# Optimization experiments

Measured on AMD Instinct MI355X. Metric: run time of the kernel, lower is better.

The kernel has to match this reference:

```python
import jax, jax.numpy as jnp
import numpy as np

EPS = 1e-5

def setup_inputs() -> dict:
    key = jax.random.key(0)
    k1, k2, k3 = jax.random.split(key, 3)
    x = jax.random.normal(k1, (16, 256, 32, 32), dtype=jnp.float32)
    embed = jax.random.normal(k2, (8192, 256), dtype=jnp.float32)
    cluster_size = jax.random.uniform(k3, (8192,), dtype=jnp.float32)
    return {"x": x, "embed": embed, "cluster_size": cluster_size}

def reference(x, embed, cluster_size):
    # x: (b, c, h, w) -> (b, h*w, c); project_in is Identity (codebook_dim == dim, heads=1)
    b, c, h, w = x.shape
    xt = jnp.transpose(x, (0, 2, 3, 1)).reshape(b, h * w, c)   # (b, n, d)
    flat = xt.reshape(-1, c)                                    # (N, d)
    d2 = (jnp.sum(flat * flat, axis=1, keepdims=True)
          - 2.0 * flat @ embed.T
          + jnp.sum(embed * embed, axis=1))                     # (N, K)
    embed_ind_flat = jnp.argmin(d2, axis=-1)                    # (N,) temperature==0 -> argmax of -d2
    quantize = embed[embed_ind_flat].reshape(b, h * w, c)       # gather codebook rows
    embed_ind = embed_ind_flat.reshape(b, h * w)
    # perplexity over (unnormalized) EMA cluster sizes, as in the torch code
    probs = cluster_size
    perplexity = jnp.exp(-jnp.sum(probs * jnp.log(probs + EPS)))
    # eval-mode commitment loss (weight_loss=True, commitment_weight=1.0)
    commit_loss = jnp.mean((quantize - xt) ** 2)
    return quantize, embed_ind, perplexity, commit_loss
```

## Files before the change

kernel.cpp:

```cpp
#include <hip/hip_runtime.h>
#include <hip/hip_bf16.h>
#include <math.h>

typedef _Float16 f16x8 __attribute__((ext_vector_type(8)));
typedef float f32x4 __attribute__((ext_vector_type(4)));

#define N_TOK 16384
#define D 256
#define K 8192

#define Q_OFF 0
#define IND_OFF 4194304
#define PERP_OFF 4210688
#define COMMIT_OFF 4210689

#define WS_CAND   0u
#define WS_E2     1048576u
#define WS_DSUM   1081344u
#define WS_EH     1114112u
#define WS_XH     5308416u
#define WS_XT     13697024u
#define WS_NEED   30474240u

__device__ __forceinline__ unsigned int ford(float f) {
    unsigned int u = __float_as_uint(f);
    return (u & 0x80000000u) ? ~u : (u | 0x80000000u);
}
__device__ __forceinline__ unsigned short f2h(float f) {
    _Float16 h = (_Float16)f;
    return *(unsigned short*)&h;
}
__device__ __forceinline__ void gload16(const void* g, void* l) {
    __builtin_amdgcn_global_load_lds(
        (const __attribute__((address_space(1))) unsigned int*)g,
        (__attribute__((address_space(3))) unsigned int*)l, 16, 0, 0);
}


__global__ void vq_convert_x(const float* __restrict__ x, float* __restrict__ xt,
                             unsigned short* __restrict__ xh) {
    __shared__ float t[64][65];
    const int tid = threadIdx.x;
    const int p0 = blockIdx.x * 64, c0 = blockIdx.y * 64, b = blockIdx.z;
    const int q = tid & 15, h = tid >> 4;
    #pragma unroll
    for (int r = 0; r < 4; ++r) {
        const int cl = r * 16 + h;
        const float4 v = *(const float4*)(x + (((size_t)(b * 256 + c0 + cl)) << 10) + p0 + q * 4);
        t[cl][q * 4 + 0] = v.x; t[cl][q * 4 + 1] = v.y;
        t[cl][q * 4 + 2] = v.z; t[cl][q * 4 + 3] = v.w;
    }
    __syncthreads();
    #pragma unroll
    for (int r = 0; r < 4; ++r) {
        const int nl = r * 16 + h;
        const int n = (b << 10) + p0 + nl;
        const int c = c0 + q * 4;
        float4 vf; ushort4 vh;
        vf.x = t[q * 4 + 0][nl]; vf.y = t[q * 4 + 1][nl];
        vf.z = t[q * 4 + 2][nl]; vf.w = t[q * 4 + 3][nl];
        vh.x = f2h(vf.x); vh.y = f2h(vf.y); vh.z = f2h(vf.z); vh.w = f2h(vf.w);
        *(float4*)(xt + ((size_t)n << 8) + c) = vf;
        *(ushort4*)(xh + ((size_t)n << 8) + c) = vh;
    }
}

__global__ void vq_prep_e(const float* __restrict__ e, unsigned short* __restrict__ eh,
                          float* __restrict__ e2, double* __restrict__ dsum) {
    if (blockIdx.x == 0 && threadIdx.x == 0) *dsum = 0.0;
    const int wave = threadIdx.x >> 6, lane = threadIdx.x & 63;
    const int c = blockIdx.x * 4 + wave;
    const float4 v = *(const float4*)(e + (size_t)c * D + lane * 4);
    ushort4 vh;
    vh.x = f2h(v.x); vh.y = f2h(v.y); vh.z = f2h(v.z); vh.w = f2h(v.w);
    *(ushort4*)(eh + (size_t)c * D + lane * 4) = vh;
    float s = v.x * v.x + v.y * v.y + v.z * v.z + v.w * v.w;
    #pragma unroll
    for (int off = 32; off > 0; off >>= 1) s += __shfl_down(s, off, 64);
    if (lane == 0) e2[c] = s;
}

__global__ __launch_bounds__(256, 2) void vq_mfma_kernel(
    const unsigned short* __restrict__ xh, const unsigned short* __restrict__ eh,
    const float* __restrict__ e2, unsigned int* __restrict__ cand) {
    __shared__ __align__(16) unsigned short Bs[2][32 * 64];

    const int tid = threadIdx.x;
    const int lane = tid & 63, wid = tid >> 6;
    const int l15 = lane & 15, lg = lane >> 4;
    const int split = blockIdx.y;
    const int m0 = blockIdx.x * 256;
    const int c0s = split * 1024;
    const int rw = m0 + wid * 64;

    f16x8 a[4][8];
    #pragma unroll
    for (int mf = 0; mf < 4; ++mf) {
        const unsigned short* ap = xh + (((size_t)(rw + mf * 16 + l15)) << 8) + lg * 8;
        #pragma unroll
        for (int t = 0; t < 8; ++t)
            a[mf][t] = *(const f16x8*)(ap + t * 32);
    }

    {
        const int r = tid >> 3, cl = tid & 7;
        gload16(eh + (((size_t)(c0s + r)) << 8) + ((cl ^ (r & 7)) << 3),
                (char*)Bs[0] + tid * 16);
    }

    int boff[2][2];
    #pragma unroll
    for (int nf = 0; nf < 2; ++nf)
        #pragma unroll
        for (int ks2 = 0; ks2 < 2; ++ks2) {
            const int rb = nf * 16 + l15;
            boff[nf][ks2] = rb * 128 + (((ks2 * 4 + lg) ^ (rb & 7)) << 4);
        }

    float d1[16], d2[16];
    unsigned int ipk[16];
    #pragma unroll
    for (int r = 0; r < 16; ++r) { d1[r] = INFINITY; d2[r] = INFINITY; ipk[r] = 0; }

    __syncthreads();

    #pragma unroll 1
    for (int ct = 0; ct < 32; ++ct) {
        const int c0 = c0s + ct * 32;
        float e2v0 = e2[c0 + l15];
        float e2v1 = e2[c0 + 16 + l15];
        f32x4 acc[4][2];
        #pragma unroll
        for (int mf = 0; mf < 4; ++mf) {
            f32x4 z = {0.f, 0.f, 0.f, 0.f};
            acc[mf][0] = z; acc[mf][1] = z;
        }
        #pragma unroll
        for (int ks = 0; ks < 4; ++ks) {
            const int s = ct * 4 + ks;
            const int cur = s & 1;
            if (s < 127) {
                const int s1 = s + 1;
                const int c0n = c0s + (s1 >> 2) * 32;
                const int kkn = (s1 & 3) * 64;
                const int r = tid >> 3, cl = tid & 7;
                gload16(eh + (((size_t)(c0n + r)) << 8) + kkn + ((cl ^ (r & 7)) << 3),
                        (char*)Bs[cur ^ 1] + tid * 16);
            }
            #pragma unroll
            for (int ks2 = 0; ks2 < 2; ++ks2) {
                const f16x8 b0 = *(const f16x8*)((const char*)Bs[cur] + boff[0][ks2]);
                const f16x8 b1 = *(const f16x8*)((const char*)Bs[cur] + boff[1][ks2]);
                #pragma unroll
                for (int mf = 0; mf < 4; ++mf) {
                    acc[mf][0] = __builtin_amdgcn_mfma_f32_16x16x32_f16(
                        a[mf][ks * 2 + ks2], b0, acc[mf][0], 0, 0, 0);
                    acc[mf][1] = __builtin_amdgcn_mfma_f32_16x16x32_f16(
                        a[mf][ks * 2 + ks2], b1, acc[mf][1], 0, 0, 0);
                }
            }
            __syncthreads();
        }
        const unsigned int cl0 = (unsigned int)(ct * 32 + l15);
        #pragma unroll
        for (int mf = 0; mf < 4; ++mf) {
            #pragma unroll
            for (int reg = 0; reg < 4; ++reg) {
                const int rr = mf * 4 + reg;
                const float sc0 = fmaf(-2.0f, acc[mf][0][reg], e2v0);
                const float sc1 = fmaf(-2.0f, acc[mf][1][reg], e2v1);
                if (fminf(sc0, sc1) < d2[rr]) {
                    {
                        const bool lt1 = sc0 < d1[rr], lt2 = sc0 < d2[rr];
                        const unsigned int ii = ipk[rr];
                        const unsigned int nif = (ii << 16) | cl0;
                        const unsigned int nis = (ii & 0xFFFFu) | (cl0 << 16);
                        d2[rr] = lt1 ? d1[rr] : (lt2 ? sc0 : d2[rr]);
                        ipk[rr] = lt1 ? nif : (lt2 ? nis : ii);
                        d1[rr] = lt1 ? sc0 : d1[rr];
                    }
                    {
                        const unsigned int cl1 = cl0 + 16;
                        const bool lt1 = sc1 < d1[rr], lt2 = sc1 < d2[rr];
                        const unsigned int ii = ipk[rr];
                        const unsigned int nif = (ii << 16) | cl1;
                        const unsigned int nis = (ii & 0xFFFFu) | (cl1 << 16);
                        d2[rr] = lt1 ? d1[rr] : (lt2 ? sc1 : d2[rr]);
                        ipk[rr] = lt1 ? nif : (lt2 ? nis : ii);
                        d1[rr] = lt1 ? sc1 : d1[rr];
                    }
                }
            }
        }
    }

    unsigned long long p1[16], p2[16];
    #pragma unroll
    for (int r = 0; r < 16; ++r) {
        p1[r] = (((unsigned long long)ford(d1[r])) << 32) |
                (unsigned int)(c0s + (ipk[r] & 0xFFFFu));
        p2[r] = (((unsigned long long)ford(d2[r])) << 32) |
                (unsigned int)(c0s + (ipk[r] >> 16));
    }
    #pragma unroll
    for (int st = 1; st < 16; st <<= 1) {
        #pragma unroll
        for (int r = 0; r < 16; ++r) {
            const unsigned long long q1 = __shfl_xor(p1[r], st, 64);
            const unsigned long long q2 = __shfl_xor(p2[r], st, 64);
            const unsigned long long n1 = p1[r] < q1 ? p1[r] : q1;
            const unsigned long long hi = p1[r] < q1 ? q1 : p1[r];
            const unsigned long long l2 = p2[r] < q2 ? p2[r] : q2;
            p1[r] = n1;
            p2[r] = hi < l2 ? hi : l2;
        }
    }
    if (l15 == 0) {
        #pragma unroll
        for (int mf = 0; mf < 4; ++mf)
            #pragma unroll
            for (int reg = 0; reg < 4; ++reg) {
                const int n = rw + mf * 16 + lg * 4 + reg;
                unsigned int* cp = cand + (((size_t)n) << 4) + split * 2;
                cp[0] = (unsigned int)p1[mf * 4 + reg];
                cp[1] = (unsigned int)p2[mf * 4 + reg];
            }
    }
}

__global__ void vq_rescore_finalize(const float* __restrict__ xt, const float* __restrict__ embed,
                                    const float* __restrict__ e2,
                                    const unsigned int* __restrict__ cand,
                                    float* __restrict__ out, double* __restrict__ dsum) {
    __shared__ double red[4];
    const int tid = threadIdx.x, wid = tid >> 6, lane = tid & 63;
    double wsum = 0.0;
    #pragma unroll 1
    for (int it = 0; it < 8; ++it) {
        const int n = blockIdx.x * 32 + it * 4 + wid;
        const float4 xv = *(const float4*)(xt + (((size_t)n) << 8) + lane * 4);
        unsigned long long best = 0xFFFFFFFFFFFFFFFFull;
        #pragma unroll 2
        for (int j = 0; j < 16; ++j) {
            const unsigned int c = cand[(((size_t)n) << 4) + j];
            const float4 ev = *(const float4*)(embed + (((size_t)c) << 8) + lane * 4);
            float dt = xv.x * ev.x + xv.y * ev.y + xv.z * ev.z + xv.w * ev.w;
            #pragma unroll
            for (int off = 32; off > 0; off >>= 1) dt += __shfl_xor(dt, off, 64);
            const float s = fmaf(-2.0f, dt, e2[c]);
            const unsigned long long p = (((unsigned long long)ford(s)) << 32) | c;
            best = p < best ? p : best;
        }
        const unsigned int bi = (unsigned int)(best & 0xFFFFFFFFull);
        if (lane == 0) out[IND_OFF + n] = (float)bi;
        const float4 ev = *(const float4*)(embed + (((size_t)bi) << 8) + lane * 4);
        *(float4*)(out + Q_OFF + (((size_t)n) << 8) + lane * 4) = ev;
        const float q0 = ev.x - xv.x, q1 = ev.y - xv.y, q2 = ev.z - xv.z, q3 = ev.w - xv.w;
        float a4 = q0 * q0 + q1 * q1 + q2 * q2 + q3 * q3;
        #pragma unroll
        for (int off = 32; off > 0; off >>= 1) a4 += __shfl_xor(a4, off, 64);
        if (lane == 0) wsum += (double)a4;
    }
    if (lane == 0) red[wid] = wsum;
    __syncthreads();
    if (tid == 0) atomicAdd(dsum, red[0] + red[1] + red[2] + red[3]);
}

__global__ void vq_tail_kernel(const float* __restrict__ cs,
                               const double* __restrict__ dsum,
                               float* __restrict__ out) {
    __shared__ double red[4];
    const int tid = threadIdx.x;
    double s = 0.0;
    for (int i = tid; i < K; i += 256) {
        const float p = cs[i];
        s += (double)(p * logf(p + 1e-5f));
    }
    #pragma unroll
    for (int off = 32; off > 0; off >>= 1) s += __shfl_down(s, off, 64);
    if ((tid & 63) == 0) red[tid >> 6] = s;
    __syncthreads();
    if (tid == 0) {
        const double tot = red[0] + red[1] + red[2] + red[3];
        const double pv = exp(-tot);
        out[PERP_OFF] = (pv > 3.3e38) ? 3.3e38f : (float)pv;
        out[COMMIT_OFF] = (float)(*dsum * (1.0 / 4194304.0));
    }
}

#define TM 64
#define TN 64
#define BKF 32
#define NSPLITF 2
#define CODES_PER_SPLIT (K / NSPLITF)
#define TILES_PER_SPLIT (CODES_PER_SPLIT / TN)

__global__ void vq_init_kernel(unsigned long long* __restrict__ keys, double* __restrict__ dsum) {
    int i = blockIdx.x * blockDim.x + threadIdx.x;
    if (i < N_TOK) keys[i] = 0xFFFFFFFFFFFFFFFFull;
    if (i == 0) *dsum = 0.0;
}
__global__ void vq_e2_kernel(const float* __restrict__ embed, float* __restrict__ e2) {
    int wave = threadIdx.x >> 6, lane = threadIdx.x & 63;
    int c = blockIdx.x * 4 + wave;
    const float4 v = *(const float4*)(embed + (size_t)c * D + lane * 4);
    float s = v.x * v.x + v.y * v.y + v.z * v.z + v.w * v.w;
    #pragma unroll
    for (int off = 32; off > 0; off >>= 1) s += __shfl_down(s, off, 64);
    if (lane == 0) e2[c] = s;
}
__global__ __launch_bounds__(256, 2) void vq_argmin_kernel(
    const float* __restrict__ x, const float* __restrict__ embed,
    const float* __restrict__ e2, unsigned long long* __restrict__ keys) {
    __shared__ float xT[D][TM];
    __shared__ float eT[BKF][TN + 4];
    const int tid = threadIdx.x;
    const int n0 = blockIdx.x * TM;
    const int b = n0 >> 10, p0 = n0 & 1023;
    const float* xb = x + (size_t)b * D * 1024 + p0;
    {
        const int t4 = (tid & 15) * 4, chb = tid >> 4;
        #pragma unroll
        for (int pass = 0; pass < 16; ++pass) {
            const int ch = pass * 16 + chb;
            *(float4*)&xT[ch][t4] = *(const float4*)(xb + (size_t)ch * 1024 + t4);
        }
    }
    __syncthreads();
    const int tm4 = (tid & 15) * 4, tn = tid >> 4, tn4 = tn * 4;
    float bestd[4]; int besti[4];
    #pragma unroll
    for (int i = 0; i < 4; ++i) { bestd[i] = INFINITY; besti[i] = 0x7fffffff; }
    for (int ct = 0; ct < TILES_PER_SPLIT; ++ct) {
        const int c0 = blockIdx.y * CODES_PER_SPLIT + ct * TN;
        float acc[4][4] = {};
        for (int kk = 0; kk < D; kk += BKF) {
            {
                const int j = tid >> 2, ch4 = (tid & 3) * 4;
                #pragma unroll
                for (int p = 0; p < 2; ++p) {
                    const int chl = p * 16 + ch4;
                    const float4 ev = *(const float4*)(embed + (size_t)(c0 + j) * D + kk + chl);
                    eT[chl + 0][j] = ev.x; eT[chl + 1][j] = ev.y;
                    eT[chl + 2][j] = ev.z; eT[chl + 3][j] = ev.w;
                }
            }
            __syncthreads();
            #pragma unroll
            for (int k2 = 0; k2 < BKF; ++k2) {
                const float4 a = *(const float4*)&xT[kk + k2][tm4];
                const float4 bv = *(const float4*)&eT[k2][tn4];
                acc[0][0] += a.x * bv.x; acc[0][1] += a.x * bv.y; acc[0][2] += a.x * bv.z; acc[0][3] += a.x * bv.w;
                acc[1][0] += a.y * bv.x; acc[1][1] += a.y * bv.y; acc[1][2] += a.y * bv.z; acc[1][3] += a.y * bv.w;
                acc[2][0] += a.z * bv.x; acc[2][1] += a.z * bv.y; acc[2][2] += a.z * bv.z; acc[2][3] += a.z * bv.w;
                acc[3][0] += a.w * bv.x; acc[3][1] += a.w * bv.y; acc[3][2] += a.w * bv.z; acc[3][3] += a.w * bv.w;
            }
            __syncthreads();
        }
        #pragma unroll
        for (int j = 0; j < 4; ++j) {
            const int c = c0 + tn4 + j;
            const float ec = e2[c];
            #pragma unroll
            for (int i = 0; i < 4; ++i) {
                const float s = ec - 2.0f * acc[i][j];
                if (s < bestd[i]) { bestd[i] = s; besti[i] = c; }
            }
        }
    }
    __syncthreads();
    float* cd = &eT[0][0];
    int* ci = (int*)&eT[16][0];
    #pragma unroll
    for (int i = 0; i < 4; ++i) { cd[tn * 64 + tm4 + i] = bestd[i]; ci[tn * 64 + tm4 + i] = besti[i]; }
    __syncthreads();
    if (tid < TM) {
        float bd = INFINITY; int bi = 0x7fffffff;
        for (int j = 0; j < 16; ++j) {
            const float d = cd[j * 64 + tid]; const int idx = ci[j * 64 + tid];
            if (d < bd || (d == bd && idx < bi)) { bd = d; bi = idx; }
        }
        atomicMin(&keys[n0 + tid], (((unsigned long long)ford(bd)) << 32) | (unsigned int)bi);
    }
}
__global__ void vq_finalize_kernel(const float* __restrict__ x, const float* __restrict__ embed,
                                   const unsigned long long* __restrict__ keys,
                                   float* __restrict__ out, double* __restrict__ dsum) {
    const int tid = threadIdx.x;
    const int n0 = blockIdx.x * 64;
    const int t = tid >> 2, q = tid & 3;
    const int n = n0 + t;
    const int b = n >> 10, p = n & 1023;
    if (tid < 64) {
        const int nn = n0 + tid;
        out[IND_OFF + nn] = (float)(int)(unsigned int)(keys[nn] & 0xFFFFFFFFull);
    }
    const int idx = (int)(unsigned int)(keys[n] & 0xFFFFFFFFull);
    const float* erow = embed + (size_t)idx * D;
    const float* xrow = x + (size_t)b * D * 1024 + p;
    float* qrow = out + Q_OFF + (size_t)n * D;
    float acc = 0.0f;
    #pragma unroll
    for (int i = 0; i < 16; ++i) {
        const int ch = i * 16 + q * 4;
        const float4 ev = *(const float4*)(erow + ch);
        *(float4*)(qrow + ch) = ev;
        const float x0 = xrow[(size_t)(ch + 0) * 1024];
        const float x1 = xrow[(size_t)(ch + 1) * 1024];
        const float x2 = xrow[(size_t)(ch + 2) * 1024];
        const float x3 = xrow[(size_t)(ch + 3) * 1024];
        const float d0 = ev.x - x0, d1 = ev.y - x1, d2 = ev.z - x2, d3 = ev.w - x3;
        acc += d0 * d0 + d1 * d1 + d2 * d2 + d3 * d3;
    }
    #pragma unroll
    for (int off = 32; off > 0; off >>= 1) acc += __shfl_down(acc, off, 64);
    if ((tid & 63) == 0) atomicAdd(dsum, (double)acc);
}

extern "C" void kernel_launch(void* const* d_in, const int* in_sizes, int n_in,
                              void* d_out, int out_size, void* d_ws, size_t ws_size,
                              hipStream_t stream) {
    const float* x = (const float*)d_in[0];
    const float* embed = (const float*)d_in[1];
    const float* cs = (const float*)d_in[2];
    float* out = (float*)d_out;
    char* ws = (char*)d_ws;

    if (ws_size >= (size_t)WS_NEED) {
        unsigned int* cand = (unsigned int*)(ws + WS_CAND);
        float* e2 = (float*)(ws + WS_E2);
        double* dsum = (double*)(ws + WS_DSUM);
        unsigned short* eh = (unsigned short*)(ws + WS_EH);
        unsigned short* xh = (unsigned short*)(ws + WS_XH);
        float* xt = (float*)(ws + WS_XT);

        vq_prep_e<<<dim3(K / 4), dim3(256), 0, stream>>>(embed, eh, e2, dsum);
        vq_convert_x<<<dim3(16, 4, 16), dim3(256), 0, stream>>>(x, xt, xh);
        vq_mfma_kernel<<<dim3(64, 8), dim3(256), 0, stream>>>(xh, eh, e2, cand);
        vq_rescore_finalize<<<dim3(512), dim3(256), 0, stream>>>(xt, embed, e2, cand, out, dsum);
        vq_tail_kernel<<<dim3(1), dim3(256), 0, stream>>>(cs, dsum, out);
    } else {
        unsigned long long* keys = (unsigned long long*)ws;
        float* e2 = (float*)(ws + 131072);
        double* dsum = (double*)(ws + 163840);
        vq_init_kernel<<<dim3(64), dim3(256), 0, stream>>>(keys, dsum);
        vq_e2_kernel<<<dim3(K / 4), dim3(256), 0, stream>>>(embed, e2);
        vq_argmin_kernel<<<dim3(N_TOK / TM, NSPLITF), dim3(256), 0, stream>>>(x, embed, e2, keys);
        vq_finalize_kernel<<<dim3(256), dim3(256), 0, stream>>>(x, embed, keys, out, dsum);
        vq_tail_kernel<<<dim3(1), dim3(256), 0, stream>>>(cs, dsum, out);
    }
}
```

Baseline: 188.0 us.

## Give each wave private triple-buffered codebook tiles and drop block barriers

Each wave now loads its own copy of the codebook tiles into a private 3-stage LDS ring buffer, prefetching two stages ahead. Per-wave vmcnt waits replace the block-wide __syncthreads. The block's e2 slice is staged once in shared memory, and MFMA sections run at raised priority. This removes barrier stalls and deepens load/compute overlap, at the cost of four times the global/L2 traffic for B tiles and more LDS per block (about 49KB for the B ring alone), which could limit occupancy.

```diff
diff --git a/kernel.cpp b/kernel.cpp
--- a/kernel.cpp
+++ b/kernel.cpp
@@ -83,7 +83,8 @@
 __global__ __launch_bounds__(256, 2) void vq_mfma_kernel(
     const unsigned short* __restrict__ xh, const unsigned short* __restrict__ eh,
     const float* __restrict__ e2, unsigned int* __restrict__ cand) {
-    __shared__ __align__(16) unsigned short Bs[2][32 * 64];
+    __shared__ __align__(16) unsigned short Bs[4][3][2048];
+    __shared__ float e2s[1024];
 
     const int tid = threadIdx.x;
     const int lane = tid & 63, wid = tid >> 6;
@@ -92,6 +93,10 @@
     const int m0 = blockIdx.x * 256;
     const int c0s = split * 1024;
     const int rw = m0 + wid * 64;
+    char* wb = (char*)&Bs[wid][0][0];
+
+    *(float4*)&e2s[tid * 4] = *(const float4*)(e2 + c0s + tid * 4);
+    __syncthreads();
 
     f16x8 a[4][8];
     #pragma unroll
@@ -101,12 +106,23 @@
         for (int t = 0; t < 8; ++t)
             a[mf][t] = *(const f16x8*)(ap + t * 32);
     }
-
-    {
-        const int r = tid >> 3, cl = tid & 7;
-        gload16(eh + (((size_t)(c0s + r)) << 8) + ((cl ^ (r & 7)) << 3),
-                (char*)Bs[0] + tid * 16);
-    }
+    #pragma unroll
+    for (int mf = 0; mf < 4; ++mf)
+        #pragma unroll
+        for (int t = 0; t < 8; ++t)
+            asm volatile("" : "+v"(*(f32x4*)&a[mf][t]));
+
+    auto stage = [&](int s, int bo) {
+        const int c0 = c0s + (s >> 2) * 32;
+        const int kk = (s & 3) * 64;
+        #pragma unroll
+        for (int i = 0; i < 4; ++i) {
+            const int chunk = i * 64 + lane;
+            const int r = chunk >> 3, cl = chunk & 7;
+            gload16(eh + (((size_t)(c0 + r)) << 8) + kk + ((cl ^ (r & 7)) << 3),
+                    wb + bo + i * 1024);
+        }
+    };
 
     int boff[2][2];
     #pragma unroll
@@ -122,13 +138,14 @@
     #pragma unroll
     for (int r = 0; r < 16; ++r) { d1[r] = INFINITY; d2[r] = INFINITY; ipk[r] = 0; }
 
-    __syncthreads();
+    int bo0 = 0, bo1 = 4096, bo2 = 8192;
+    stage(0, bo0);
+    stage(1, bo1);
 
     #pragma unroll 1
     for (int ct = 0; ct < 32; ++ct) {
-        const int c0 = c0s + ct * 32;
-        float e2v0 = e2[c0 + l15];
-        float e2v1 = e2[c0 + 16 + l15];
+        const float e2v0 = e2s[ct * 32 + l15];
+        const float e2v1 = e2s[ct * 32 + 16 + l15];
         f32x4 acc[4][2];
         #pragma unroll
         for (int mf = 0; mf < 4; ++mf) {
@@ -138,19 +155,15 @@
         #pragma unroll
         for (int ks = 0; ks < 4; ++ks) {
             const int s = ct * 4 + ks;
-            const int cur = s & 1;
-            if (s < 127) {
-                const int s1 = s + 1;
-                const int c0n = c0s + (s1 >> 2) * 32;
-                const int kkn = (s1 & 3) * 64;
-                const int r = tid >> 3, cl = tid & 7;
-                gload16(eh + (((size_t)(c0n + r)) << 8) + kkn + ((cl ^ (r & 7)) << 3),
-                        (char*)Bs[cur ^ 1] + tid * 16);
-            }
+            if (s < 126) stage(s + 2, bo2);
+            if (s < 126)      asm volatile("s_waitcnt vmcnt(8)" ::: "memory");
+            else if (s == 126) asm volatile("s_waitcnt vmcnt(4)" ::: "memory");
+            else               asm volatile("s_waitcnt vmcnt(0)" ::: "memory");
+            __builtin_amdgcn_s_setprio(1);
             #pragma unroll
             for (int ks2 = 0; ks2 < 2; ++ks2) {
-                const f16x8 b0 = *(const f16x8*)((const char*)Bs[cur] + boff[0][ks2]);
-                const f16x8 b1 = *(const f16x8*)((const char*)Bs[cur] + boff[1][ks2]);
+                const f16x8 b0 = *(const f16x8*)(wb + bo0 + boff[0][ks2]);
+                const f16x8 b1 = *(const f16x8*)(wb + bo0 + boff[1][ks2]);
                 #pragma unroll
                 for (int mf = 0; mf < 4; ++mf) {
                     acc[mf][0] = __builtin_amdgcn_mfma_f32_16x16x32_f16(
@@ -159,7 +172,8 @@
                         a[mf][ks * 2 + ks2], b1, acc[mf][1], 0, 0, 0);
                 }
             }
-            __syncthreads();
+            __builtin_amdgcn_s_setprio(0);
+            const int tmp = bo0; bo0 = bo1; bo1 = bo2; bo2 = tmp;
         }
         const unsigned int cl0 = (unsigned int)(ct * 32 + l15);
         #pragma unroll
```

Result: slower. 201.9 us (+7.4%).
